# Kernel tuning notes

Hardware: AMD Instinct MI355X
Metric: run time of the kernel (lower is better)

The kernel has to match this reference:

```python
import jax, jax.numpy as jnp
import numpy as np

CPG = 2          # channels_per_group
WH, WW = 227, 227  # window_size
EPS = 1e-05


def setup_inputs() -> dict:
    key = jax.random.key(0)
    x = jax.random.normal(key, (8, 32, 512, 512), dtype=jnp.float32)
    weight = jnp.ones((1, 32, 1, 1), dtype=jnp.float32)
    bias = jnp.zeros((1, 32, 1, 1), dtype=jnp.float32)
    return {"x": x, "weight": weight, "bias": bias}


def _box_sum(ii, wh, ww):
    # ii: integral image (N,C,H,W); returns window sums of size (wh,ww)
    # over rows h+1..h+wh, cols w+1..w+ww -> (N,C,H-wh,W-ww)
    return (ii[:, :, wh:, ww:] - ii[:, :, :-wh, ww:]
            - ii[:, :, wh:, :-ww] + ii[:, :, :-wh, :-ww])


def reference(x, weight, bias):
    N, C, H, W = x.shape
    G = C // CPG
    # window_size (227,227) < (H,W)=(512,512): integral-image branch
    ii = jnp.cumsum(jnp.cumsum(x, axis=2), axis=3)
    ii_sq = jnp.cumsum(jnp.cumsum(x * x, axis=2), axis=3)
    h, w = H - WH, W - WW
    # per-channel box sums, then sum over channels_per_group -> (N,G,h,w)
    sums = _box_sum(ii, WH, WW).reshape(N, G, CPG, h, w).sum(axis=2)
    squares = _box_sum(ii_sq, WH, WW).reshape(N, G, CPG, h, w).sum(axis=2)
    n = WH * WW * CPG
    means = sums / n
    var = (squares - sums * sums / n) / n
    # replicate-pad stats back to (H,W): (left,right,top,bottom) like F.pad
    pt, pb = (H - h) // 2, H - h - (H - h) // 2
    pl, pr = (W - w) // 2, W - w - (W - w) // 2
    pad = ((0, 0), (0, 0), (pt, pb), (pl, pr))
    p_means = jnp.pad(means, pad, mode='edge')
    p_vars = jnp.pad(var, pad, mode='edge') + EPS
    # torch computes sums/squares under no_grad -> stats are constants
    p_means = jax.lax.stop_gradient(p_means)
    p_vars = jax.lax.stop_gradient(p_vars)
    xg = x.reshape(N, G, CPG, H, W)
    out = (xg - p_means[:, :, None]) / jnp.sqrt(p_vars)[:, :, None]
    out = out.reshape(N, C, H, W)
    return out * weight + bias
```

## Files before the change

kernel.cpp:

```cpp
#include <hip/hip_runtime.h>

namespace {
constexpr int Hn = 512, Wn = 512;
constexpr int WHn = 227, WWn = 227;
constexpr int OHn = Hn - WHn;
constexpr int OWn = Wn - WWn;
constexpr int PTn = 113, PLn = 113;
constexpr float EPSn = 1e-5f;
}

__global__ __launch_bounds__(512, 4) void lcn_fused(const float* __restrict__ x,
                                                    const float* __restrict__ weight,
                                                    const float* __restrict__ bias,
                                                    float* __restrict__ out) {
  const int blk = blockIdx.x;
  const int chunk = blk & 3;
  const int g = blk >> 2;
  const int w = threadIdx.x;
  const int lane = w & 63;
  const int wid = w >> 6;

  const float* __restrict__ x0 = x + (size_t)(g * 2) * Hn * Wn;
  const float* __restrict__ x1 = x0 + (size_t)Hn * Wn;
  float* __restrict__ o0 = out + (size_t)(g * 2) * Hn * Wn;
  float* __restrict__ o1 = o0 + (size_t)Hn * Wn;
  const int cch = (g & 15) * 2;
  const float wt0 = weight[cch], wt1 = weight[cch + 1];
  const float bs0 = bias[cch], bs1 = bias[cch + 1];

  const int h0 = chunk == 0 ? 0 : chunk == 1 ? 44 : chunk == 2 ? 144 : 244;
  const int h1 = chunk == 0 ? 44 : chunk == 1 ? 144 : chunk == 2 ? 244 : 285;

  __shared__ __align__(16) float2 Ps[4][Wn + 1];
  __shared__ float2 wsum[8][4];
  __shared__ float2 bstat[4][132];

  const int q = w & 127;
  const int p = w >> 7;
  float4 sS = {0.f, 0.f, 0.f, 0.f}, sQ = {0.f, 0.f, 0.f, 0.f};
  {
    const float4* __restrict__ r0 =
        reinterpret_cast<const float4*>(x0 + (size_t)(h0 + 1) * Wn) + q;
    const float4* __restrict__ r1 =
        reinterpret_cast<const float4*>(x1 + (size_t)(h0 + 1) * Wn) + q;
    #pragma unroll 8
    for (int r = p; r < WHn; r += 4) {
      float4 a = r0[(size_t)r * (Wn / 4)];
      float4 b = r1[(size_t)r * (Wn / 4)];
      sS.x += a.x + b.x; sQ.x += a.x * a.x + b.x * b.x;
      sS.y += a.y + b.y; sQ.y += a.y * a.y + b.y * b.y;
      sS.z += a.z + b.z; sQ.z += a.z * a.z + b.z * b.z;
      sS.w += a.w + b.w; sQ.w += a.w * a.w + b.w * b.w;
    }
  }
  float accS, accQ;
  {
    float4* cc = reinterpret_cast<float4*>(&Ps[0][0]);
    cc[p * 256 + 2 * q]     = make_float4(sS.x, sQ.x, sS.y, sQ.y);
    cc[p * 256 + 2 * q + 1] = make_float4(sS.z, sQ.z, sS.w, sQ.w);
    __syncthreads();
    const float2* cf = reinterpret_cast<const float2*>(&Ps[0][0]);
    float2 t0 = cf[0 * Wn + w], t1 = cf[1 * Wn + w];
    float2 t2 = cf[2 * Wn + w], t3 = cf[3 * Wn + w];
    accS = (t0.x + t1.x) + (t2.x + t3.x);
    accQ = (t0.y + t1.y) + (t2.y + t3.y);
    __syncthreads();
  }

  const float inv_n = 1.0f / (float)(WHn * WWn * 2);
  const int wp = min(max(w - PLn, 0), OWn - 1);

  float pa0[4], pa1[4], ps0[4], ps1[4];
  auto prefetch = [&](int hb) {
    #pragma unroll
    for (int j = 0; j < 4; ++j) {
      int ra = min(hb + WHn + 1 + j, Hn - 1);
      int rs = hb + 1 + j;
      pa0[j] = x0[(size_t)ra * Wn + w];
      pa1[j] = x1[(size_t)ra * Wn + w];
      ps0[j] = x0[(size_t)rs * Wn + w];
      ps1[j] = x1[(size_t)rs * Wn + w];
    }
  };
  prefetch(h0);

  for (int h = h0; h < h1; h += 4) {
    float2 v[4];
    v[0] = make_float2(accS, accQ);
    float s2 = accS, q2 = accQ;
    #pragma unroll
    for (int j = 0; j < 3; ++j) {
      s2 += (pa0[j] + pa1[j]) - (ps0[j] + ps1[j]);
      q2 += (pa0[j] * pa0[j] + pa1[j] * pa1[j])
          - (ps0[j] * ps0[j] + ps1[j] * ps1[j]);
      v[j + 1] = make_float2(s2, q2);
    }
    s2 += (pa0[3] + pa1[3]) - (ps0[3] + ps1[3]);
    q2 += (pa0[3] * pa0[3] + pa1[3] * pa1[3])
        - (ps0[3] * ps0[3] + ps1[3] * ps1[3]);
    accS = s2; accQ = q2;

    if (h + 4 < h1) prefetch(h + 4);
    float xa[4], xb[4];
    #pragma unroll
    for (int rr = 0; rr < 4; ++rr) {
      const size_t hh = (size_t)(h + PTn + rr) * Wn + w;
      xa[rr] = x0[hh];
      xb[rr] = x1[hh];
    }

    #pragma unroll
    for (int d = 1; d < 64; d <<= 1) {
      #pragma unroll
      for (int rr = 0; rr < 4; ++rr) {
        float sx = __shfl_up(v[rr].x, d, 64);
        float sy = __shfl_up(v[rr].y, d, 64);
        if (lane >= d) { v[rr].x += sx; v[rr].y += sy; }
      }
    }
    if (lane == 63) {
      #pragma unroll
      for (int rr = 0; rr < 4; ++rr) wsum[wid][rr] = v[rr];
    }
    __syncthreads();
    float2 off[4] = {{0.f,0.f},{0.f,0.f},{0.f,0.f},{0.f,0.f}};
    #pragma unroll
    for (int i = 0; i < 7; ++i) {
      if (i < wid) {
        #pragma unroll
        for (int rr = 0; rr < 4; ++rr) {
          off[rr].x += wsum[i][rr].x; off[rr].y += wsum[i][rr].y;
        }
      }
    }
    #pragma unroll
    for (int rr = 0; rr < 4; ++rr)
      Ps[rr][w + 1] = make_float2(v[rr].x + off[rr].x, v[rr].y + off[rr].y);
    __syncthreads();

    #pragma unroll
    for (int rr = 0; rr < 4; ++rr) {
      if (h + rr < h1) {
        float2 hi = Ps[rr][wp + WWn + 1];
        float2 lo = Ps[rr][wp + 1];
        float S = hi.x - lo.x;
        float Q = hi.y - lo.y;
        float mean = S * inv_n;
        float var = (Q - S * S * inv_n) * inv_n;
        float istd = rsqrtf(var + EPSn);
        if (rr == 0 && ((chunk == 0 && h == 0) || (chunk == 3 && h == 284)))
          bstat[w & 3][w >> 2] = make_float2(mean, istd);
        const size_t oo = (size_t)(h + PTn + rr) * Wn + w;
        o0[oo] = (xa[rr] - mean) * istd * wt0 + bs0;
        o1[oo] = (xb[rr] - mean) * istd * wt1 + bs1;
      }
    }
    __syncthreads();
  }

  if (chunk == 0 || chunk == 3) {
    const int row0 = (chunk == 0) ? 0 : 398;
    const int nrows = (chunk == 0) ? PTn : Hn - 398;
    const int total = nrows * 256;
    const float4* __restrict__ xf0 = reinterpret_cast<const float4*>(x0);
    const float4* __restrict__ xf1 = reinterpret_cast<const float4*>(x1);
    float4* __restrict__ of0 = reinterpret_cast<float4*>(o0);
    float4* __restrict__ of1 = reinterpret_cast<float4*>(o1);
    for (int i = w; i < total; i += 512) {
      const int qq = i & 127;
      const int ch = (i >> 7) & 1;
      const int row = row0 + (i >> 8);
      const size_t idx = (size_t)row * (Wn / 4) + qq;
      const float4 xv = ch ? xf1[idx] : xf0[idx];
      const float wt = ch ? wt1 : wt0;
      const float bsv = ch ? bs1 : bs0;
      const float2 m0 = bstat[0][qq];
      const float2 m1 = bstat[1][qq];
      const float2 m2 = bstat[2][qq];
      const float2 m3 = bstat[3][qq];
      float4 ov;
      ov.x = (xv.x - m0.x) * m0.y * wt + bsv;
      ov.y = (xv.y - m1.x) * m1.y * wt + bsv;
      ov.z = (xv.z - m2.x) * m2.y * wt + bsv;
      ov.w = (xv.w - m3.x) * m3.y * wt + bsv;
      if (ch) of1[idx] = ov; else of0[idx] = ov;
    }
  }
}

extern "C" void kernel_launch(void* const* d_in, const int* in_sizes, int n_in,
                              void* d_out, int out_size, void* d_ws, size_t ws_size,
                              hipStream_t stream) {
  const float* x = (const float*)d_in[0];
  const float* weight = (const float*)d_in[1];
  const float* bias = (const float*)d_in[2];
  float* out = (float*)d_out;

  hipLaunchKernelGGL(lcn_fused, dim3(128 * 4), dim3(512), 0, stream,
                     x, weight, bias, out);
}
```

Before: 204.4 us.

## Precompute per-chunk column-sum snapshots and split sliding window into eight chunks

```diff
diff --git a/kernel.cpp b/kernel.cpp
--- a/kernel.cpp
+++ b/kernel.cpp
@@ -3,19 +3,83 @@
 namespace {
 constexpr int Hn = 512, Wn = 512;
 constexpr int WHn = 227, WWn = 227;
-constexpr int OHn = Hn - WHn;
-constexpr int OWn = Wn - WWn;
+constexpr int OHn = 285, OWn = 285;
 constexpr int PTn = 113, PLn = 113;
 constexpr float EPSn = 1e-5f;
-}
-
-__global__ __launch_bounds__(512, 4) void lcn_fused(const float* __restrict__ x,
+constexpr int NSEG = 17, NSLOT = 9;
+__device__ __constant__ int kSegA[NSEG] =
+    {1,37,73,109,145,181,217,228,253,264,285,300,336,372,408,444,480};
+__device__ __constant__ int kSegB[NSEG] =
+    {36,72,108,144,180,216,227,252,263,284,299,335,371,407,443,479,511};
+__device__ __constant__ int kWinLo[NSLOT] = {0,1,2,3,4,5,6,8,10};
+__device__ __constant__ int kWinHi[NSLOT] = {6,8,10,11,12,13,14,15,16};
+__device__ __constant__ int kBr0[8] = {0,29,57,85,398,427,456,484};
+__device__ __constant__ int kBrN[8] = {29,28,28,28,29,29,28,28};
+}
+
+__global__ __launch_bounds__(512, 4) void lcn_snap(const float* __restrict__ x,
+                                                   float2* __restrict__ snap) {
+  const int B = blockIdx.x;
+  const int g = B >> 2;
+  const int st = B & 3;
+  const int w = threadIdx.x;
+  const int q2 = w & 31;
+  const int p = w >> 5;
+
+  const float4* __restrict__ b0 =
+      reinterpret_cast<const float4*>(x + (size_t)(g * 2) * Hn * Wn) + st * 32 + q2;
+  const float4* __restrict__ b1 = b0 + (size_t)Hn * (Wn / 4);
+
+  __shared__ float4 tbuf[16][64];
+  __shared__ float2 segLds[NSEG][128];
+
+  for (int s = 0; s < NSEG; ++s) {
+    float4 aS = {0.f,0.f,0.f,0.f}, aQ = {0.f,0.f,0.f,0.f};
+    for (int r = kSegA[s] + p; r <= kSegB[s]; r += 16) {
+      float4 a = b0[(size_t)r * (Wn / 4)];
+      float4 b = b1[(size_t)r * (Wn / 4)];
+      aS.x += a.x + b.x; aQ.x += a.x * a.x + b.x * b.x;
+      aS.y += a.y + b.y; aQ.y += a.y * a.y + b.y * b.y;
+      aS.z += a.z + b.z; aQ.z += a.z * a.z + b.z * b.z;
+      aS.w += a.w + b.w; aQ.w += a.w * a.w + b.w * b.w;
+    }
+    __syncthreads();
+    tbuf[p][2 * q2]     = make_float4(aS.x, aQ.x, aS.y, aQ.y);
+    tbuf[p][2 * q2 + 1] = make_float4(aS.z, aQ.z, aS.w, aQ.w);
+    __syncthreads();
+    if (w < 128) {
+      const float2* cf = reinterpret_cast<const float2*>(&tbuf[0][0]);
+      float2 acc = {0.f, 0.f};
+      #pragma unroll
+      for (int pp = 0; pp < 16; ++pp) {
+        float2 t = cf[pp * 128 + w];
+        acc.x += t.x; acc.y += t.y;
+      }
+      segLds[s][w] = acc;
+    }
+  }
+  __syncthreads();
+  if (w < 128) {
+    for (int k = 0; k < NSLOT; ++k) {
+      float2 acc = {0.f, 0.f};
+      for (int i = kWinLo[k]; i <= kWinHi[k]; ++i) {
+        acc.x += segLds[i][w].x; acc.y += segLds[i][w].y;
+      }
+      snap[((size_t)g * NSLOT + k) * 512 + st * 128 + w] = acc;
+    }
+  }
+}
+
+__global__ __launch_bounds__(512, 8) void lcn_fused(const float* __restrict__ x,
                                                     const float* __restrict__ weight,
                                                     const float* __restrict__ bias,
+                                                    const float2* __restrict__ snap,
                                                     float* __restrict__ out) {
-  const int blk = blockIdx.x;
-  const int chunk = blk & 3;
-  const int g = blk >> 2;
+  const int B = blockIdx.x;
+  const int X = B & 7;
+  const int s = B >> 3;
+  const int chunk = s & 7;
+  const int g = X * 16 + (s >> 3);
   const int w = threadIdx.x;
   const int lane = w & 63;
   const int wid = w >> 6;
@@ -28,44 +92,16 @@
   const float wt0 = weight[cch], wt1 = weight[cch + 1];
   const float bs0 = bias[cch], bs1 = bias[cch + 1];
 
-  const int h0 = chunk == 0 ? 0 : chunk == 1 ? 44 : chunk == 2 ? 144 : 244;
-  const int h1 = chunk == 0 ? 44 : chunk == 1 ? 144 : chunk == 2 ? 244 : 285;
-
-  __shared__ __align__(16) float2 Ps[4][Wn + 1];
+  const int h0 = chunk * 36;
+  const int h1 = min(OHn, h0 + 36);
+
+  __shared__ __align__(16) float2 Ps[2][4][Wn + 1];
   __shared__ float2 wsum[8][4];
-  __shared__ float2 bstat[4][132];
-
-  const int q = w & 127;
-  const int p = w >> 7;
-  float4 sS = {0.f, 0.f, 0.f, 0.f}, sQ = {0.f, 0.f, 0.f, 0.f};
-  {
-    const float4* __restrict__ r0 =
-        reinterpret_cast<const float4*>(x0 + (size_t)(h0 + 1) * Wn) + q;
-    const float4* __restrict__ r1 =
-        reinterpret_cast<const float4*>(x1 + (size_t)(h0 + 1) * Wn) + q;
-    #pragma unroll 8
-    for (int r = p; r < WHn; r += 4) {
-      float4 a = r0[(size_t)r * (Wn / 4)];
-      float4 b = r1[(size_t)r * (Wn / 4)];
-      sS.x += a.x + b.x; sQ.x += a.x * a.x + b.x * b.x;
-      sS.y += a.y + b.y; sQ.y += a.y * a.y + b.y * b.y;
-      sS.z += a.z + b.z; sQ.z += a.z * a.z + b.z * b.z;
-      sS.w += a.w + b.w; sQ.w += a.w * a.w + b.w * b.w;
-    }
-  }
-  float accS, accQ;
-  {
-    float4* cc = reinterpret_cast<float4*>(&Ps[0][0]);
-    cc[p * 256 + 2 * q]     = make_float4(sS.x, sQ.x, sS.y, sQ.y);
-    cc[p * 256 + 2 * q + 1] = make_float4(sS.z, sQ.z, sS.w, sQ.w);
-    __syncthreads();
-    const float2* cf = reinterpret_cast<const float2*>(&Ps[0][0]);
-    float2 t0 = cf[0 * Wn + w], t1 = cf[1 * Wn + w];
-    float2 t2 = cf[2 * Wn + w], t3 = cf[3 * Wn + w];
-    accS = (t0.x + t1.x) + (t2.x + t3.x);
-    accQ = (t0.y + t1.y) + (t2.y + t3.y);
-    __syncthreads();
-  }
+
+  const float2 sv = snap[((size_t)g * NSLOT + chunk) * 512 + w];
+  float accS = sv.x, accQ = sv.y;
+  const int bslot = (chunk < 4) ? 0 : 8;
+  const float2 bv = snap[((size_t)g * NSLOT + bslot) * 512 + w];
 
   const float inv_n = 1.0f / (float)(WHn * WWn * 2);
   const int wp = min(max(w - PLn, 0), OWn - 1);
@@ -84,6 +120,7 @@
   };
   prefetch(h0);
 
+  int buf = 0;
   for (int h = h0; h < h1; h += 4) {
     float2 v[4];
     v[0] = make_float2(accS, accQ);
@@ -135,33 +172,59 @@
     }
     #pragma unroll
     for (int rr = 0; rr < 4; ++rr)
-      Ps[rr][w + 1] = make_float2(v[rr].x + off[rr].x, v[rr].y + off[rr].y);
+      Ps[buf][rr][w + 1] = make_float2(v[rr].x + off[rr].x, v[rr].y + off[rr].y);
     __syncthreads();
 
     #pragma unroll
     for (int rr = 0; rr < 4; ++rr) {
       if (h + rr < h1) {
-        float2 hi = Ps[rr][wp + WWn + 1];
-        float2 lo = Ps[rr][wp + 1];
+        float2 hi = Ps[buf][rr][wp + WWn + 1];
+        float2 lo = Ps[buf][rr][wp + 1];
         float S = hi.x - lo.x;
         float Q = hi.y - lo.y;
         float mean = S * inv_n;
         float var = (Q - S * S * inv_n) * inv_n;
         float istd = rsqrtf(var + EPSn);
-        if (rr == 0 && ((chunk == 0 && h == 0) || (chunk == 3 && h == 284)))
-          bstat[w & 3][w >> 2] = make_float2(mean, istd);
         const size_t oo = (size_t)(h + PTn + rr) * Wn + w;
         o0[oo] = (xa[rr] - mean) * istd * wt0 + bs0;
         o1[oo] = (xb[rr] - mean) * istd * wt1 + bs1;
       }
     }
-    __syncthreads();
-  }
-
-  if (chunk == 0 || chunk == 3) {
-    const int row0 = (chunk == 0) ? 0 : 398;
-    const int nrows = (chunk == 0) ? PTn : Hn - 398;
-    const int total = nrows * 256;
+    buf ^= 1;
+  }
+
+  __syncthreads();
+  {
+    float2 v = bv;
+    #pragma unroll
+    for (int d = 1; d < 64; d <<= 1) {
+      float sx = __shfl_up(v.x, d, 64);
+      float sy = __shfl_up(v.y, d, 64);
+      if (lane >= d) { v.x += sx; v.y += sy; }
+    }
+    if (lane == 63) wsum[wid][0] = v;
+    __syncthreads();
+    float2 off = {0.f, 0.f};
+    #pragma unroll
+    for (int i = 0; i < 7; ++i) {
+      if (i < wid) { off.x += wsum[i][0].x; off.y += wsum[i][0].y; }
+    }
+    Ps[0][0][w + 1] = make_float2(v.x + off.x, v.y + off.y);
+    __syncthreads();
+    float2 hi = Ps[0][0][wp + WWn + 1];
+    float2 lo = Ps[0][0][wp + 1];
+    float S = hi.x - lo.x;
+    float Q = hi.y - lo.y;
+    float mean = S * inv_n;
+    float var = (Q - S * S * inv_n) * inv_n;
+    float istd = rsqrtf(var + EPSn);
+    Ps[0][1][w] = make_float2(mean, istd);
+    __syncthreads();
+  }
+  {
+    const float2* bst = &Ps[0][1][0];
+    const int row0 = kBr0[chunk];
+    const int total = kBrN[chunk] * 256;
     const float4* __restrict__ xf0 = reinterpret_cast<const float4*>(x0);
     const float4* __restrict__ xf1 = reinterpret_cast<const float4*>(x1);
     float4* __restrict__ of0 = reinterpret_cast<float4*>(o0);
@@ -174,10 +237,10 @@
       const float4 xv = ch ? xf1[idx] : xf0[idx];
       const float wt = ch ? wt1 : wt0;
       const float bsv = ch ? bs1 : bs0;
-      const float2 m0 = bstat[0][qq];
-      const float2 m1 = bstat[1][qq];
-      const float2 m2 = bstat[2][qq];
-      const float2 m3 = bstat[3][qq];
+      const float2 m0 = bst[4 * qq + 0];
+      const float2 m1 = bst[4 * qq + 1];
+      const float2 m2 = bst[4 * qq + 2];
+      const float2 m3 = bst[4 * qq + 3];
       float4 ov;
       ov.x = (xv.x - m0.x) * m0.y * wt + bsv;
       ov.y = (xv.y - m1.x) * m1.y * wt + bsv;
@@ -195,7 +258,9 @@
   const float* weight = (const float*)d_in[1];
   const float* bias = (const float*)d_in[2];
   float* out = (float*)d_out;
-
-  hipLaunchKernelGGL(lcn_fused, dim3(128 * 4), dim3(512), 0, stream,
-                     x, weight, bias, out);
-}
+  float2* snap = (float2*)d_ws;
+
+  hipLaunchKernelGGL(lcn_snap, dim3(512), dim3(512), 0, stream, x, snap);
+  hipLaunchKernelGGL(lcn_fused, dim3(1024), dim3(512), 0, stream,
+                     x, weight, bias, snap, out);
+}
```

New measurement: 232.4 us. 13.7% more time.
